# Kernel optimization log

Measured on AMD Instinct MI355X. Metric: run time of the kernel, lower is better.

The kernel has to match this reference:

```python
import jax, jax.numpy as jnp
import numpy as np

B, T, IN, H, F = 512, 32, 8, 64, 1
IN1 = IN + F  # input_size + feats


def setup_inputs() -> dict:
    key = jax.random.key(0)
    ks = jax.random.split(key, 8)
    s = 0.05
    return {
        "input_data": jax.random.normal(ks[0], (B, T, IN), jnp.float32),
        "y_prev": jax.random.normal(ks[1], (B, T), jnp.float32),
        "Wv": jax.random.normal(ks[2], (H, H + IN1), jnp.float32) * s,
        "bv": jnp.zeros((H,), jnp.float32),
        "W_ih": jax.random.normal(ks[3], (4 * H, IN1), jnp.float32) * s,
        "W_hh": jax.random.normal(ks[4], (4 * H, H), jnp.float32) * s,
        "b_ih": jnp.zeros((4 * H,), jnp.float32),
        "b_hh": jnp.zeros((4 * H,), jnp.float32),
        "Wp": jax.random.normal(ks[5], (1, H + IN1), jnp.float32) * s,
        "bp": jnp.zeros((1,), jnp.float32),
        "Wf": jax.random.normal(ks[6], (F, H), jnp.float32) * s,
        "bf": jnp.zeros((F,), jnp.float32),
        "num_particles": 256,
    }


def _forward(input_data, y_prev, Wv, bv, W_ih, W_hh, b_ih, b_hh, Wp, bp, Wf, bf, num_particles):
    b, t_len, _ = input_data.shape
    h_dim = Wf.shape[1]
    P = num_particles
    noise_key = jax.random.key(1234)

    new_input = jnp.concatenate([input_data, y_prev[:, :, None]], axis=2)  # [B,T,IN1]
    xs = jnp.moveaxis(new_input, 1, 0)  # [T,B,IN1]
    h0 = jnp.zeros((P, b, h_dim), input_data.dtype)
    c0 = jnp.zeros((P, b, h_dim), input_data.dtype)

    def step(carry, xt_t):
        h, c = carry  # each [P,B,H], particle-major
        x_t, t = xt_t  # [B,IN1], scalar t
        hidden_mean = h.mean(axis=0)  # [B,H] (mean over particles)
        var = jnp.concatenate([x_t, hidden_mean], axis=1) @ Wv.T + bv  # [B,H]
        std = jax.nn.softplus(var)
        # single LSTM cell step over P*B "batch" rows (input tiled over particles)
        gates = x_t @ W_ih.T + b_ih + h @ W_hh.T + b_hh  # [P,B,4H]
        i, f, g, o = jnp.split(gates, 4, axis=-1)  # torch gate order i,f,g,o
        c_new = jax.nn.sigmoid(f) * c + jax.nn.sigmoid(i) * jnp.tanh(g)
        h_lstm = jax.nn.sigmoid(o) * jnp.tanh(c_new)
        # reparameterize: mu + eps*std (std broadcast over particle dim)
        eps = jax.random.normal(jax.random.fold_in(noise_key, t), (P, b, h_dim), h.dtype)
        h_rep = h_lstm + eps * std
        # sort_hidden: per batch element, reorder particles by fc_final projection
        proj = (h_rep @ Wf.T + bf)[..., 0]  # [P,B]
        order = jnp.argsort(proj, axis=0)  # [P,B]
        h_sorted = jnp.take_along_axis(h_rep, order[:, :, None], axis=0)
        y = jnp.concatenate([h_sorted, jnp.broadcast_to(x_t, (P, b, x_t.shape[1]))], axis=-1)
        logpdf = (y @ Wp.T + bp)[..., 0]  # [P,B]
        # faithful to torch's view(-1, P, 1) on a particle-major flat buffer
        pr = logpdf.reshape(-1).reshape(b, P)
        w_inc = jnp.exp(pr).mean(axis=1, keepdims=True)  # [B,1]
        return (h_sorted, c_new), w_inc

    (h_fin, _), w_incs = jax.lax.scan(step, (h0, c0), (xs, jnp.arange(t_len)))
    weights = w_incs.sum(axis=0)  # [B,1]
    y_pred = h_fin.mean(axis=0) @ Wf.T + bf  # [B,1]
    return y_pred, weights


def reference(input_data, y_prev, Wv, bv, W_ih, W_hh, b_ih, b_hh, Wp, bp, Wf, bf, num_particles):
    return _forward(input_data, y_prev, Wv, bv, W_ih, W_hh, b_ih, b_hh, Wp, bp, Wf, bf, num_particles)
```

## Files before the change

kernel.cpp:

```cpp
#include <hip/hip_runtime.h>
#include <stdint.h>

#define NB 512
#define NT 32
#define NIN 8
#define NIN1 9
#define NH 64
#define NP 256
#define NTHR 512
#define HROW 68

typedef __attribute__((ext_vector_type(8))) _Float16 f16x8;
typedef __attribute__((ext_vector_type(16))) float f32x16;

struct FKeys { uint32_t a[NT]; uint32_t b[NT]; };

__host__ __device__ __forceinline__ void tfr(uint32_t& x0, uint32_t& x1, int r) {
  x0 += x1; x1 = (x1 << r) | (x1 >> (32 - r)); x1 ^= x0;
}

__host__ __device__ __forceinline__ void threefry2x32(uint32_t k0, uint32_t k1,
                                                      uint32_t& x0, uint32_t& x1) {
  uint32_t k2 = k0 ^ k1 ^ 0x1BD11BDAu;
  x0 += k0; x1 += k1;
  tfr(x0,x1,13); tfr(x0,x1,15); tfr(x0,x1,26); tfr(x0,x1,6);
  x0 += k1; x1 += k2 + 1u;
  tfr(x0,x1,17); tfr(x0,x1,29); tfr(x0,x1,16); tfr(x0,x1,24);
  x0 += k2; x1 += k0 + 2u;
  tfr(x0,x1,13); tfr(x0,x1,15); tfr(x0,x1,26); tfr(x0,x1,6);
  x0 += k0; x1 += k1 + 3u;
  tfr(x0,x1,17); tfr(x0,x1,29); tfr(x0,x1,16); tfr(x0,x1,24);
  x0 += k1; x1 += k2 + 4u;
  tfr(x0,x1,13); tfr(x0,x1,15); tfr(x0,x1,26); tfr(x0,x1,6);
  x0 += k2; x1 += k0 + 5u;
}

__device__ __forceinline__ float normal_from_bits(uint32_t bits) {
  float f = __uint_as_float((bits >> 9) | 0x3f800000u) - 1.0f;
  const float lo = -0.99999994f;
  float u = fmaxf(lo, fmaf(f, 2.0f, lo));
  float w = -__logf(fmaf(-u, u, 1.0f));
  float p;
  if (w < 5.0f) {
    w -= 2.5f;
    p = 2.81022636e-08f;
    p = fmaf(p, w, 3.43273939e-07f);
    p = fmaf(p, w, -3.5233877e-06f);
    p = fmaf(p, w, -4.39150654e-06f);
    p = fmaf(p, w, 0.00021858087f);
    p = fmaf(p, w, -0.00125372503f);
    p = fmaf(p, w, -0.00417768164f);
    p = fmaf(p, w, 0.246640727f);
    p = fmaf(p, w, 1.50140941f);
  } else {
    w = sqrtf(w) - 3.0f;
    p = -0.000200214257f;
    p = fmaf(p, w, 0.000100950558f);
    p = fmaf(p, w, 0.00134934322f);
    p = fmaf(p, w, -0.00367342844f);
    p = fmaf(p, w, 0.00573950773f);
    p = fmaf(p, w, -0.0076224613f);
    p = fmaf(p, w, 0.00943887047f);
    p = fmaf(p, w, 1.00167406f);
    p = fmaf(p, w, 2.83297682f);
  }
  return 1.41421356f * (p * u);
}

__device__ __forceinline__ float frcp(float x) { return __builtin_amdgcn_rcpf(x); }
__device__ __forceinline__ float fsigmoid(float x) { return frcp(1.0f + __expf(-x)); }
__device__ __forceinline__ float ftanh(float x) { return 1.0f - 2.0f * frcp(1.0f + __expf(2.0f * x)); }

__device__ __forceinline__ uint32_t pack_f16(float x) {
  union { _Float16 h; uint16_t u; } c;
  c.h = (_Float16)x;
  return (uint32_t)c.u;
}

__device__ __forceinline__ f16x8 ld8h(const _Float16* p) {
  union { f16x8 v; uint64_t q[2]; } u;
  u.q[0] = *(const uint64_t*)(p);
  u.q[1] = *(const uint64_t*)(p + 4);
  return u.v;
}

__global__ __launch_bounds__(NTHR, 2)
void pf_main(const float* __restrict__ input_data, const float* __restrict__ y_prev,
             const float* __restrict__ Wv, const float* __restrict__ bv,
             const float* __restrict__ W_ih, const float* __restrict__ W_hh,
             const float* __restrict__ b_ih, const float* __restrict__ b_hh,
             const float* __restrict__ Wp, const float* __restrict__ bp,
             const float* __restrict__ Wf, const float* __restrict__ bf,
             float* __restrict__ out, float* __restrict__ gw,
             FKeys fk)
{
  __shared__ __align__(16) _Float16 h1_s[NP * HROW];
  __shared__ __align__(16) _Float16 h0_s[NP * HROW];
  __shared__ __align__(16) float xg_s[NP];
  __shared__ __align__(16) float proj_s[NP];
  __shared__ float lp_s[NP];
  __shared__ float wsum_s[NP];
  __shared__ int   rankP_s[2 * NP];
  __shared__ float hsum_s[NH];
  __shared__ float std_s[NH];
  __shared__ float xs_s[16];

  const int tid  = threadIdx.x;
  const int b    = blockIdx.x;
  const int lane = tid & 63;
  const int wq   = tid >> 6;
  const int ln31 = lane & 31;
  const int h5   = lane >> 5;

  for (int i = tid; i < NP * HROW; i += NTHR) h1_s[i] = (_Float16)0.0f;
  if (tid < NP) wsum_s[tid] = 0.0f;
  if (tid < NH) hsum_s[tid] = 0.0f;

  const float bf0 = bf[0];
  const float bp0 = bp[0];
  const uint32_t bsh = (uint32_t)b << 6;

  const int rp   = 32 * wq + ln31;
  const int orig = (rp & 3) * NH + (rp >> 2);
  f16x8 w1f[4];
  #pragma unroll
  for (int kt = 0; kt < 4; ++kt) {
    #pragma unroll
    for (int e = 0; e < 8; ++e)
      w1f[kt][e] = (_Float16)W_hh[orig * NH + kt * 16 + h5 * 8 + e];
  }

  float wf_r[4], wp_r[4];
  #pragma unroll
  for (int q = 0; q < 4; ++q) {
    const int kq = 8 * wq + 2 * q + h5;
    wf_r[q] = Wf[kq];
    wp_r[q] = Wp[kq];
  }

  float cA[4][4], cB[4][4];
  #pragma unroll
  for (int mi = 0; mi < 4; ++mi) {
    #pragma unroll
    for (int q = 0; q < 4; ++q) { cA[mi][q] = 0.0f; cB[mi][q] = 0.0f; }
  }

  auto finalize_init = [&]() {
    if (tid < NH) {
      float v = bv[tid];
      const float* wvr = Wv + tid * (NIN1 + NH);
      #pragma unroll
      for (int i = 0; i < NIN1; ++i) v = fmaf(xs_s[i], wvr[i], v);
      #pragma unroll
      for (int k = 0; k < NH; ++k)
        v = fmaf(hsum_s[k] * (1.0f / NP), wvr[NIN1 + k], v);
      std_s[tid] = fmaxf(v, 0.0f) + log1pf(expf(-fabsf(v)));
    }
    if (tid < NP) {
      const int orow = (tid & 3) * NH + (tid >> 2);
      float a = b_ih[orow] + b_hh[orow];
      const float* wr = W_ih + orow * NIN1;
      #pragma unroll
      for (int i = 0; i < NIN1; ++i) a = fmaf(xs_s[i], wr[i], a);
      xg_s[tid] = a;
      proj_s[tid] = bf0;
      float xp = bp0;
      #pragma unroll
      for (int i = 0; i < NIN1; ++i) xp = fmaf(xs_s[i], Wp[NH + i], xp);
      lp_s[tid] = xp;
    }
  };

  if (tid < NIN) xs_s[tid] = input_data[(b * NT + 0) * NIN + tid];
  if (tid == NIN) xs_s[NIN] = y_prev[b * NT + 0];
  __syncthreads();
  finalize_init();
  __syncthreads();

  for (int t = 0; t < NT; ++t) {
    if (tid < 16 && t + 1 < NT) {
      if (tid < NIN) xs_s[tid] = input_data[(b * NT + t + 1) * NIN + tid];
      if (tid == NIN) xs_s[NIN] = y_prev[b * NT + t + 1];
    }

    float std_r[4];
    #pragma unroll
    for (int q = 0; q < 4; ++q) std_r[q] = std_s[8 * wq + 2 * q + h5];

    const uint32_t fk0 = fk.a[t], fk1 = fk.b[t];
    float hs[4] = {0.0f, 0.0f, 0.0f, 0.0f};

    #pragma unroll
    for (int mi = 0; mi < 4; ++mi) {
      const int pA = mi * 32 + ln31;

      f32x16 acc;
      #pragma unroll
      for (int q = 0; q < 4; ++q) {
        const float4 v = *(const float4*)&xg_s[32 * wq + 8 * q + 4 * h5];
        acc[4 * q + 0] = v.x; acc[4 * q + 1] = v.y;
        acc[4 * q + 2] = v.z; acc[4 * q + 3] = v.w;
      }
      #pragma unroll
      for (int kt = 0; kt < 4; ++kt) {
        const f16x8 b1 = ld8h(&h1_s[pA * HROW + kt * 16 + h5 * 8]);
        acc = __builtin_amdgcn_mfma_f32_32x32x16_f16(w1f[kt], b1, acc, 0, 0, 0);
      }
      float hlA[4];
      #pragma unroll
      for (int q = 0; q < 4; ++q) {
        float si = fsigmoid(acc[4 * q + 0]);
        float sf = fsigmoid(acc[4 * q + 1]);
        float so = fsigmoid(acc[4 * q + 3]);
        float cn = sf * cA[mi][q] + si * ftanh(acc[4 * q + 2]);
        cA[mi][q] = cn;
        hlA[q] = so * ftanh(cn);
      }
      #pragma unroll
      for (int q = 0; q < 4; ++q) {
        const float4 v = *(const float4*)&xg_s[32 * wq + 8 * q + 4 * h5];
        acc[4 * q + 0] = v.x; acc[4 * q + 1] = v.y;
        acc[4 * q + 2] = v.z; acc[4 * q + 3] = v.w;
      }
      #pragma unroll
      for (int kt = 0; kt < 4; ++kt) {
        const f16x8 b1 = ld8h(&h1_s[(pA + 128) * HROW + kt * 16 + h5 * 8]);
        acc = __builtin_amdgcn_mfma_f32_32x32x16_f16(w1f[kt], b1, acc, 0, 0, 0);
      }
      float plA = 0.0f, lpA = 0.0f, plB = 0.0f, lpB = 0.0f;
      uint32_t sh[4];
      #pragma unroll
      for (int q = 0; q < 4; ++q) {
        const int kq = 8 * wq + 2 * q + h5;
        float si = fsigmoid(acc[4 * q + 0]);
        float sf = fsigmoid(acc[4 * q + 1]);
        float so = fsigmoid(acc[4 * q + 3]);
        float cnB = sf * cB[mi][q] + si * ftanh(acc[4 * q + 2]);
        cB[mi][q] = cnB;
        float hlB = so * ftanh(cnB);
        uint32_t x0 = ((uint32_t)pA << 15) | bsh | (uint32_t)kq;
        uint32_t x1 = x0 + (1u << 22);
        threefry2x32(fk0, fk1, x0, x1);
        float hA = fmaf(normal_from_bits(x0), std_r[q], hlA[q]);
        float hB = fmaf(normal_from_bits(x1), std_r[q], hlB);
        hs[q] += hA + hB;
        plA = fmaf(hA, wf_r[q], plA); lpA = fmaf(hA, wp_r[q], lpA);
        plB = fmaf(hB, wf_r[q], plB); lpB = fmaf(hB, wp_r[q], lpB);
        const uint32_t pkA = pack_f16(hA);
        const uint32_t pkB = pack_f16(hB);
        const uint32_t send = h5 ? pkA : pkB;
        const uint32_t got  = (uint32_t)__shfl_xor((int)send, 32, 64);
        const uint32_t ev = h5 ? got : pkA;
        const uint32_t od = h5 ? pkB : got;
        sh[q] = (ev & 0xffffu) | (od << 16);
      }
      {
        const int row = pA + (h5 ? 128 : 0);
        _Float16* d = &h0_s[row * HROW + 8 * wq];
        *(uint64_t*)(d)     = (uint64_t)sh[0] | ((uint64_t)sh[1] << 32);
        *(uint64_t*)(d + 4) = (uint64_t)sh[2] | ((uint64_t)sh[3] << 32);
      }
      plA += __shfl_xor(plA, 32, 64); lpA += __shfl_xor(lpA, 32, 64);
      plB += __shfl_xor(plB, 32, 64); lpB += __shfl_xor(lpB, 32, 64);
      if (lane < 32) {
        atomicAdd(&proj_s[pA], plA);
        atomicAdd(&lp_s[pA], lpA);
        atomicAdd(&proj_s[pA + 128], plB);
        atomicAdd(&lp_s[pA + 128], lpB);
      }
    }
    #pragma unroll
    for (int q = 0; q < 4; ++q) {
      float s = hs[q];
      s += __shfl_xor(s, 1, 64); s += __shfl_xor(s, 2, 64); s += __shfl_xor(s, 4, 64);
      s += __shfl_xor(s, 8, 64); s += __shfl_xor(s, 16, 64);
      if (ln31 == q) hsum_s[8 * wq + 2 * q + h5] = s;
    }
    __syncthreads();

    {
      const int ph = tid & (NP - 1);
      const int hh = tid >> 8;
      const float pv = proj_s[ph];
      int rk = 0;
      const float4* c4 = (const float4*)proj_s;
      #pragma unroll 8
      for (int q4 = 32 * hh; q4 < 32 * hh + 32; ++q4) {
        float4 v = c4[q4];
        int qb = q4 * 4;
        rk += (v.x < pv || (v.x == pv && qb + 0 < ph)) ? 1 : 0;
        rk += (v.y < pv || (v.y == pv && qb + 1 < ph)) ? 1 : 0;
        rk += (v.z < pv || (v.z == pv && qb + 2 < ph)) ? 1 : 0;
        rk += (v.w < pv || (v.w == pv && qb + 3 < ph)) ? 1 : 0;
      }
      rankP_s[hh * NP + ph] = rk;
    }
    __syncthreads();

    {
      const int ph = tid & (NP - 1);
      const int hh = tid >> 8;
      const int rank = rankP_s[ph] + rankP_s[NP + ph];
      const uint64_t* s = (const uint64_t*)&h0_s[ph * HROW + 32 * hh];
      const uint64_t v0 = s[0], v1 = s[1], v2 = s[2], v3 = s[3];
      uint64_t* d = (uint64_t*)&h1_s[rank * HROW + 32 * hh];
      d[0] = v0; d[1] = v1; d[2] = v2; d[3] = v3;
      if (hh == 0) wsum_s[rank] += __expf(lp_s[ph]);
    }
    finalize_init();
    __syncthreads();
  }

  if (tid < NH) {
    float hm = hsum_s[tid] * (1.0f / NP);
    float contrib = hm * Wf[tid];
    contrib += __shfl_xor(contrib, 32, 64);
    contrib += __shfl_xor(contrib, 16, 64);
    contrib += __shfl_xor(contrib, 8, 64);
    contrib += __shfl_xor(contrib, 4, 64);
    contrib += __shfl_xor(contrib, 2, 64);
    contrib += __shfl_xor(contrib, 1, 64);
    if (tid == 0) out[b] = contrib + bf0;
  }
  if (tid < NP) gw[(size_t)tid * NB + b] = wsum_s[tid];
}

__global__ __launch_bounds__(64, 1)
void pf_weights(const float* __restrict__ gw, float* __restrict__ out) {
  int i = blockIdx.x;
  int lane = threadIdx.x;
  const float* src = gw + ((size_t)(i >> 1)) * NB + (size_t)(i & 1) * NP;
  float4 v = ((const float4*)src)[lane];
  float s = (v.x + v.y) + (v.z + v.w);
  s += __shfl_xor(s, 32, 64);
  s += __shfl_xor(s, 16, 64);
  s += __shfl_xor(s, 8, 64);
  s += __shfl_xor(s, 4, 64);
  s += __shfl_xor(s, 2, 64);
  s += __shfl_xor(s, 1, 64);
  if (lane == 0) out[NB + i] = s * (1.0f / NP);
}

extern "C" void kernel_launch(void* const* d_in, const int* in_sizes, int n_in,
                              void* d_out, int out_size, void* d_ws, size_t ws_size,
                              hipStream_t stream) {
  (void)in_sizes; (void)n_in; (void)out_size; (void)ws_size;
  const float* input_data = (const float*)d_in[0];
  const float* y_prev     = (const float*)d_in[1];
  const float* Wv         = (const float*)d_in[2];
  const float* bv         = (const float*)d_in[3];
  const float* W_ih       = (const float*)d_in[4];
  const float* W_hh       = (const float*)d_in[5];
  const float* b_ih       = (const float*)d_in[6];
  const float* b_hh       = (const float*)d_in[7];
  const float* Wp         = (const float*)d_in[8];
  const float* bp         = (const float*)d_in[9];
  const float* Wf         = (const float*)d_in[10];
  const float* bf         = (const float*)d_in[11];
  float* out = (float*)d_out;
  float* gw  = (float*)d_ws;

  FKeys fk;
  for (int t = 0; t < NT; ++t) {
    uint32_t x0 = 0u, x1 = (uint32_t)t;
    threefry2x32(0u, 1234u, x0, x1);
    fk.a[t] = x0; fk.b[t] = x1;
  }

  pf_main<<<dim3(NB), dim3(NTHR), 0, stream>>>(
      input_data, y_prev, Wv, bv, W_ih, W_hh, b_ih, b_hh, Wp, bp, Wf, bf,
      out, gw, fk);
  pf_weights<<<dim3(NB), dim3(64), 0, stream>>>(gw, out);
}
```

Measured before the change: 1.343 ms.

## Switch LSTM recurrent GEMM to 16x16x32 MFMA with packed fp16 cell state

Replaces the 32x32x16 MFMA tiling of the recurrent gate GEMM with 16x16x32 MFMA tiles, remapping lanes so each lane holds one hidden unit's four gates for one particle. The cell state is stored as packed fp16 pairs in registers rather than fp32, which halves its register footprint, presumably to relieve pressure at two blocks per CU. Hidden outputs are written with scalar fp16 stores instead of shuffled 64-bit stores. Storing the cell state in fp16 loses precision across the 32 steps and may change which particles are reordered. The scalar stores also add LDS traffic.

Result: no change. 1.343 ms (+0.0%).

```diff
diff --git a/kernel.cpp b/kernel.cpp
--- a/kernel.cpp
+++ b/kernel.cpp
@@ -11,7 +11,7 @@
 #define HROW 68
 
 typedef __attribute__((ext_vector_type(8))) _Float16 f16x8;
-typedef __attribute__((ext_vector_type(16))) float f32x16;
+typedef __attribute__((ext_vector_type(4))) float f32x4;
 
 struct FKeys { uint32_t a[NT]; uint32_t b[NT]; };
 
@@ -76,6 +76,11 @@
   c.h = (_Float16)x;
   return (uint32_t)c.u;
 }
+__device__ __forceinline__ float unpk_f16(uint32_t w, int hi) {
+  union { _Float16 h; uint16_t u; } c;
+  c.u = hi ? (uint16_t)(w >> 16) : (uint16_t)(w & 0xffffu);
+  return (float)c.h;
+}
 
 __device__ __forceinline__ f16x8 ld8h(const _Float16* p) {
   union { f16x8 v; uint64_t q[2]; } u;
@@ -109,8 +114,8 @@
   const int b    = blockIdx.x;
   const int lane = tid & 63;
   const int wq   = tid >> 6;
-  const int ln31 = lane & 31;
-  const int h5   = lane >> 5;
+  const int lrow = (lane >> 4) & 3;
+  const int lcol = lane & 15;
 
   for (int i = tid; i < NP * HROW; i += NTHR) h1_s[i] = (_Float16)0.0f;
   if (tid < NP) wsum_s[tid] = 0.0f;
@@ -120,30 +125,32 @@
   const float bp0 = bp[0];
   const uint32_t bsh = (uint32_t)b << 6;
 
-  const int rp   = 32 * wq + ln31;
-  const int orig = (rp & 3) * NH + (rp >> 2);
-  f16x8 w1f[4];
+  f16x8 w1f[2][2];
   #pragma unroll
-  for (int kt = 0; kt < 4; ++kt) {
-    #pragma unroll
-    for (int e = 0; e < 8; ++e)
-      w1f[kt][e] = (_Float16)W_hh[orig * NH + kt * 16 + h5 * 8 + e];
-  }
-
-  float wf_r[4], wp_r[4];
+  for (int kg2 = 0; kg2 < 2; ++kg2) {
+    const int rpr  = 32 * wq + 16 * kg2 + lcol;
+    const int orig = (rpr & 3) * NH + (rpr >> 2);
+    #pragma unroll
+    for (int kt = 0; kt < 2; ++kt) {
+      #pragma unroll
+      for (int e = 0; e < 8; ++e)
+        w1f[kg2][kt][e] = (_Float16)W_hh[orig * NH + kt * 32 + lrow * 8 + e];
+    }
+  }
+
+  float wf2[2], wp2[2];
   #pragma unroll
-  for (int q = 0; q < 4; ++q) {
-    const int kq = 8 * wq + 2 * q + h5;
-    wf_r[q] = Wf[kq];
-    wp_r[q] = Wp[kq];
-  }
-
-  float cA[4][4], cB[4][4];
+  for (int kg2 = 0; kg2 < 2; ++kg2) {
+    const int k = 8 * wq + 4 * kg2 + lrow;
+    wf2[kg2] = Wf[k];
+    wp2[kg2] = Wp[k];
+  }
+
+  uint32_t cp[2][8];
   #pragma unroll
-  for (int mi = 0; mi < 4; ++mi) {
-    #pragma unroll
-    for (int q = 0; q < 4; ++q) { cA[mi][q] = 0.0f; cB[mi][q] = 0.0f; }
-  }
+  for (int kg2 = 0; kg2 < 2; ++kg2)
+    #pragma unroll
+    for (int j = 0; j < 8; ++j) cp[kg2][j] = 0u;
 
   auto finalize_init = [&]() {
     if (tid < NH) {
@@ -183,98 +190,74 @@
       if (tid == NIN) xs_s[NIN] = y_prev[b * NT + t + 1];
     }
 
-    float std_r[4];
-    #pragma unroll
-    for (int q = 0; q < 4; ++q) std_r[q] = std_s[8 * wq + 2 * q + h5];
+    float std2[2];
+    #pragma unroll
+    for (int kg2 = 0; kg2 < 2; ++kg2) std2[kg2] = std_s[8 * wq + 4 * kg2 + lrow];
 
     const uint32_t fk0 = fk.a[t], fk1 = fk.b[t];
-    float hs[4] = {0.0f, 0.0f, 0.0f, 0.0f};
-
-    #pragma unroll
-    for (int mi = 0; mi < 4; ++mi) {
-      const int pA = mi * 32 + ln31;
-
-      f32x16 acc;
-      #pragma unroll
-      for (int q = 0; q < 4; ++q) {
-        const float4 v = *(const float4*)&xg_s[32 * wq + 8 * q + 4 * h5];
-        acc[4 * q + 0] = v.x; acc[4 * q + 1] = v.y;
-        acc[4 * q + 2] = v.z; acc[4 * q + 3] = v.w;
-      }
-      #pragma unroll
-      for (int kt = 0; kt < 4; ++kt) {
-        const f16x8 b1 = ld8h(&h1_s[pA * HROW + kt * 16 + h5 * 8]);
-        acc = __builtin_amdgcn_mfma_f32_32x32x16_f16(w1f[kt], b1, acc, 0, 0, 0);
-      }
-      float hlA[4];
-      #pragma unroll
-      for (int q = 0; q < 4; ++q) {
-        float si = fsigmoid(acc[4 * q + 0]);
-        float sf = fsigmoid(acc[4 * q + 1]);
-        float so = fsigmoid(acc[4 * q + 3]);
-        float cn = sf * cA[mi][q] + si * ftanh(acc[4 * q + 2]);
-        cA[mi][q] = cn;
-        hlA[q] = so * ftanh(cn);
-      }
-      #pragma unroll
-      for (int q = 0; q < 4; ++q) {
-        const float4 v = *(const float4*)&xg_s[32 * wq + 8 * q + 4 * h5];
-        acc[4 * q + 0] = v.x; acc[4 * q + 1] = v.y;
-        acc[4 * q + 2] = v.z; acc[4 * q + 3] = v.w;
-      }
-      #pragma unroll
-      for (int kt = 0; kt < 4; ++kt) {
-        const f16x8 b1 = ld8h(&h1_s[(pA + 128) * HROW + kt * 16 + h5 * 8]);
-        acc = __builtin_amdgcn_mfma_f32_32x32x16_f16(w1f[kt], b1, acc, 0, 0, 0);
-      }
-      float plA = 0.0f, lpA = 0.0f, plB = 0.0f, lpB = 0.0f;
-      uint32_t sh[4];
-      #pragma unroll
-      for (int q = 0; q < 4; ++q) {
-        const int kq = 8 * wq + 2 * q + h5;
-        float si = fsigmoid(acc[4 * q + 0]);
-        float sf = fsigmoid(acc[4 * q + 1]);
-        float so = fsigmoid(acc[4 * q + 3]);
-        float cnB = sf * cB[mi][q] + si * ftanh(acc[4 * q + 2]);
-        cB[mi][q] = cnB;
-        float hlB = so * ftanh(cnB);
-        uint32_t x0 = ((uint32_t)pA << 15) | bsh | (uint32_t)kq;
+    float hs2[2] = {0.0f, 0.0f};
+
+    #pragma unroll
+    for (int pt8 = 0; pt8 < 8; ++pt8) {
+      const int p = 16 * pt8 + lcol;
+      const f16x8 bA0 = ld8h(&h1_s[p * HROW + lrow * 8]);
+      const f16x8 bA1 = ld8h(&h1_s[p * HROW + 32 + lrow * 8]);
+      const f16x8 bB0 = ld8h(&h1_s[(p + 128) * HROW + lrow * 8]);
+      const f16x8 bB1 = ld8h(&h1_s[(p + 128) * HROW + 32 + lrow * 8]);
+
+      float plp = 0.0f, lpp = 0.0f, plp1 = 0.0f, lpp1 = 0.0f;
+      #pragma unroll
+      for (int kg2 = 0; kg2 < 2; ++kg2) {
+        const int k = 8 * wq + 4 * kg2 + lrow;
+        const float4 xgv = *(const float4*)&xg_s[32 * wq + 16 * kg2 + 4 * lrow];
+        f32x4 accA, accB;
+        accA[0] = xgv.x; accA[1] = xgv.y; accA[2] = xgv.z; accA[3] = xgv.w;
+        accB = accA;
+        accA = __builtin_amdgcn_mfma_f32_16x16x32_f16(w1f[kg2][0], bA0, accA, 0, 0, 0);
+        accB = __builtin_amdgcn_mfma_f32_16x16x32_f16(w1f[kg2][0], bB0, accB, 0, 0, 0);
+        accA = __builtin_amdgcn_mfma_f32_16x16x32_f16(w1f[kg2][1], bA1, accA, 0, 0, 0);
+        accB = __builtin_amdgcn_mfma_f32_16x16x32_f16(w1f[kg2][1], bB1, accB, 0, 0, 0);
+        float si = fsigmoid(accA[0]);
+        float sf = fsigmoid(accA[1]);
+        float so = fsigmoid(accA[3]);
+        float cold = unpk_f16(cp[kg2][pt8], 0);
+        float cn = sf * cold + si * ftanh(accA[2]);
+        float hlA = so * ftanh(cn);
+        float si2 = fsigmoid(accB[0]);
+        float sf2 = fsigmoid(accB[1]);
+        float so2 = fsigmoid(accB[3]);
+        float cold2 = unpk_f16(cp[kg2][pt8], 1);
+        float cn2 = sf2 * cold2 + si2 * ftanh(accB[2]);
+        cp[kg2][pt8] = pack_f16(cn) | (pack_f16(cn2) << 16);
+        float hlB = so2 * ftanh(cn2);
+        uint32_t x0 = ((uint32_t)p << 15) | bsh | (uint32_t)k;
         uint32_t x1 = x0 + (1u << 22);
         threefry2x32(fk0, fk1, x0, x1);
-        float hA = fmaf(normal_from_bits(x0), std_r[q], hlA[q]);
-        float hB = fmaf(normal_from_bits(x1), std_r[q], hlB);
-        hs[q] += hA + hB;
-        plA = fmaf(hA, wf_r[q], plA); lpA = fmaf(hA, wp_r[q], lpA);
-        plB = fmaf(hB, wf_r[q], plB); lpB = fmaf(hB, wp_r[q], lpB);
-        const uint32_t pkA = pack_f16(hA);
-        const uint32_t pkB = pack_f16(hB);
-        const uint32_t send = h5 ? pkA : pkB;
-        const uint32_t got  = (uint32_t)__shfl_xor((int)send, 32, 64);
-        const uint32_t ev = h5 ? got : pkA;
-        const uint32_t od = h5 ? pkB : got;
-        sh[q] = (ev & 0xffffu) | (od << 16);
+        float hA = fmaf(normal_from_bits(x0), std2[kg2], hlA);
+        float hB = fmaf(normal_from_bits(x1), std2[kg2], hlB);
+        hs2[kg2] += hA + hB;
+        plp  = fmaf(hA, wf2[kg2], plp);  lpp  = fmaf(hA, wp2[kg2], lpp);
+        plp1 = fmaf(hB, wf2[kg2], plp1); lpp1 = fmaf(hB, wp2[kg2], lpp1);
+        h0_s[p * HROW + k] = (_Float16)hA;
+        h0_s[(p + 128) * HROW + k] = (_Float16)hB;
       }
-      {
-        const int row = pA + (h5 ? 128 : 0);
-        _Float16* d = &h0_s[row * HROW + 8 * wq];
-        *(uint64_t*)(d)     = (uint64_t)sh[0] | ((uint64_t)sh[1] << 32);
-        *(uint64_t*)(d + 4) = (uint64_t)sh[2] | ((uint64_t)sh[3] << 32);
+      plp  += __shfl_xor(plp, 16, 64);  plp  += __shfl_xor(plp, 32, 64);
+      lpp  += __shfl_xor(lpp, 16, 64);  lpp  += __shfl_xor(lpp, 32, 64);
+      plp1 += __shfl_xor(plp1, 16, 64); plp1 += __shfl_xor(plp1, 32, 64);
+      lpp1 += __shfl_xor(lpp1, 16, 64); lpp1 += __shfl_xor(lpp1, 32, 64);
+      if (lane < 16) {
+        atomicAdd(&proj_s[p], plp);
+        atomicAdd(&lp_s[p], lpp);
+        atomicAdd(&proj_s[p + 128], plp1);
+        atomicAdd(&lp_s[p + 128], lpp1);
       }
-      plA += __shfl_xor(plA, 32, 64); lpA += __shfl_xor(lpA, 32, 64);
-      plB += __shfl_xor(plB, 32, 64); lpB += __shfl_xor(lpB, 32, 64);
-      if (lane < 32) {
-        atomicAdd(&proj_s[pA], plA);
-        atomicAdd(&lp_s[pA], lpA);
-        atomicAdd(&proj_s[pA + 128], plB);
-        atomicAdd(&lp_s[pA + 128], lpB);
-      }
-    }
-    #pragma unroll
-    for (int q = 0; q < 4; ++q) {
-      float s = hs[q];
-      s += __shfl_xor(s, 1, 64); s += __shfl_xor(s, 2, 64); s += __shfl_xor(s, 4, 64);
-      s += __shfl_xor(s, 8, 64); s += __shfl_xor(s, 16, 64);
-      if (ln31 == q) hsum_s[8 * wq + 2 * q + h5] = s;
+    }
+    #pragma unroll
+    for (int kg2 = 0; kg2 < 2; ++kg2) {
+      float s = hs2[kg2];
+      s += __shfl_xor(s, 1, 64); s += __shfl_xor(s, 2, 64);
+      s += __shfl_xor(s, 4, 64); s += __shfl_xor(s, 8, 64);
+      if (lcol == 0) hsum_s[8 * wq + 4 * kg2 + lrow] = s;
     }
     __syncthreads();
 
```
